# Optimization experiments

Hardware: AMD Instinct MI355X
Metric: run time of the kernel (lower is better)

## Reference

```python
import jax, jax.numpy as jnp
import numpy as np

EMBED_DIM = 1024
NUM_HEADS = 16
HEAD_DIM = EMBED_DIM // NUM_HEADS


def setup_inputs() -> dict:
    key = jax.random.key(0)
    ks = jax.random.split(key, 9)
    B, S, D = 4, 2048, EMBED_DIM
    s = 1.0 / np.sqrt(D)
    return {
        "x": jax.random.normal(ks[0], (B, S, D), dtype=jnp.float32),
        "Wq": jax.random.uniform(ks[1], (D, D), jnp.float32, -s, s),
        "bq": jax.random.uniform(ks[2], (D,), jnp.float32, -s, s),
        "Wk": jax.random.uniform(ks[3], (D, D), jnp.float32, -s, s),
        "bk": jax.random.uniform(ks[4], (D,), jnp.float32, -s, s),
        "Wv": jax.random.uniform(ks[5], (D, D), jnp.float32, -s, s),
        "bv": jax.random.uniform(ks[6], (D,), jnp.float32, -s, s),
        "Wo": jax.random.uniform(ks[7], (D, D), jnp.float32, -s, s),
        "bo": jax.random.uniform(ks[8], (D,), jnp.float32, -s, s),
    }


def reference(x, Wq, bq, Wk, bk, Wv, bv, Wo, bo):
    B, S, D = x.shape
    H, Hd = NUM_HEADS, HEAD_DIM

    def proj(W, b):
        # torch Linear: x @ W.T + b; reshape to [B, H, S, Hd]
        y = jnp.einsum('bsd,ed->bse', x, W) + b
        return y.reshape(B, S, H, Hd).transpose(0, 2, 1, 3)

    Q = proj(Wq, bq)
    K = proj(Wk, bk)
    V = proj(Wv, bv)
    scores = jnp.einsum('bhqd,bhkd->bhqk', Q, K) / np.sqrt(Hd).astype(jnp.float32)
    attn = jax.nn.softmax(scores, axis=-1)
    out = jnp.einsum('bhqk,bhkd->bhqd', attn, V)
    out = out.transpose(0, 2, 1, 3).reshape(B, S, D)
    return jnp.einsum('bsd,ed->bse', out, Wo) + bo
```

## Files before the change

### kernel.cpp

```cpp
#include <hip/hip_runtime.h>
#include <stdint.h>

typedef unsigned short u16;
typedef _Float16 f16;
typedef __fp16 fp16x2 __attribute__((ext_vector_type(2)));
typedef f16 f16x8 __attribute__((ext_vector_type(8)));
typedef float f32x4 __attribute__((ext_vector_type(4)));
typedef u16 u16x8v __attribute__((ext_vector_type(8)));
typedef uint32_t u32x4 __attribute__((ext_vector_type(4)));

#define MFMAH __builtin_amdgcn_mfma_f32_16x16x32_f16

__device__ __forceinline__ void gload16(const void* g, void* l) {
    __builtin_amdgcn_global_load_lds(
        (const __attribute__((address_space(1))) uint32_t*)g,
        (__attribute__((address_space(3))) uint32_t*)l, 16, 0, 0);
}

__global__ __launch_bounds__(256) void convert_x(const float4* __restrict__ x,
                                                 f16x8* __restrict__ o) {
    int i = blockIdx.x * 256 + threadIdx.x;
    float4 a = x[2 * i], b = x[2 * i + 1];
    f16x8 h;
    h[0] = (f16)a.x; h[1] = (f16)a.y; h[2] = (f16)a.z; h[3] = (f16)a.w;
    h[4] = (f16)b.x; h[5] = (f16)b.y; h[6] = (f16)b.z; h[7] = (f16)b.w;
    o[i] = h;
}

__global__ __launch_bounds__(256) void convert_w(const float4* __restrict__ Wq,
                                                 const float4* __restrict__ Wk,
                                                 const float4* __restrict__ Wv,
                                                 const float4* __restrict__ Wo,
                                                 f16x8* __restrict__ hi,
                                                 f16x8* __restrict__ lo) {
    int gi = blockIdx.x * 256 + threadIdx.x;
    int wsel = gi >> 17;
    int li = gi & 131071;
    const float4* src = (wsel == 0) ? Wq : (wsel == 1) ? Wk : (wsel == 2) ? Wv : Wo;
    float4 a = src[2 * li], b = src[2 * li + 1];
    float v[8] = {a.x, a.y, a.z, a.w, b.x, b.y, b.z, b.w};
    f16x8 h;
#pragma unroll
    for (int j = 0; j < 8; ++j) h[j] = (f16)v[j];
    hi[gi] = h;
    if (wsel == 3) {
        f16x8 l;
#pragma unroll
        for (int j = 0; j < 8; ++j) l[j] = (f16)(v[j] - (float)h[j]);
        lo[gi] = l;
    }
}

__global__ __launch_bounds__(512, 4)
void gemm_qkv(const f16* __restrict__ A,
              const f16* __restrict__ Whi,
              const float* __restrict__ b0, const float* __restrict__ b1,
              const float* __restrict__ b2,
              f16* __restrict__ oq, f16* __restrict__ ok, f16* __restrict__ ov) {
    __shared__ f16 ldsA[256 * 64];
    __shared__ f16 ldsW[128 * 64];
    const int t = threadIdx.x;
    const int lane = t & 63, quad = lane >> 4, l16 = lane & 15;
    const int wid = t >> 6;
    const int wsel = blockIdx.x >> 3;
    const int bm = blockIdx.y * 256;
    const int bn = (blockIdx.x & 7) * 128;
    const int wm = (wid >> 1) * 64, wn = (wid & 1) * 64;
    const f16* Wh = Whi + (size_t)wsel * 1048576;
    const float* bias = (wsel == 0) ? b0 : (wsel == 1) ? b1 : b2;

    f32x4 acc[4][4] = {};

    for (int kt = 0; kt < 16; ++kt) {
        __syncthreads();
        const int k0 = kt * 64;
#pragma unroll
        for (int c = 0; c < 4; ++c) {
            const int u = c * 512 + t;
            const int r = u >> 3, cc = u & 7;
            const int sc = cc ^ (r & 7);
            gload16(A + (size_t)(bm + r) * 1024 + k0 + sc * 8, &ldsA[u * 8]);
        }
#pragma unroll
        for (int c = 0; c < 2; ++c) {
            const int u = c * 512 + t;
            const int r = u >> 3, cc = u & 7;
            const int sc = cc ^ (r & 7);
            gload16(Wh + (size_t)(bn + r) * 1024 + k0 + sc * 8, &ldsW[u * 8]);
        }
        __syncthreads();

#pragma unroll
        for (int kq = 0; kq < 2; ++kq) {
            f16x8 bh[4];
            const int chb = kq * 4 + quad;
            const int ch = chb ^ (l16 & 7);
#pragma unroll
            for (int i = 0; i < 4; ++i) {
                const int rb = wn + i * 16 + l16;
                bh[i] = *(const f16x8*)&ldsW[rb * 64 + ch * 8];
            }
#pragma unroll
            for (int mi = 0; mi < 4; ++mi) {
                const int ra = wm + mi * 16 + l16;
                const f16x8 af = *(const f16x8*)&ldsA[ra * 64 + ch * 8];
#pragma unroll
                for (int ni = 0; ni < 4; ++ni)
                    acc[mi][ni] = MFMAH(af, bh[ni], acc[mi][ni], 0, 0, 0);
            }
        }
    }

#pragma unroll
    for (int ni = 0; ni < 4; ++ni) {
        const int e = bn + wn + ni * 16 + l16;
        const float bv = bias[e];
        const int h = e >> 6, d = e & 63;
#pragma unroll
        for (int mi = 0; mi < 4; ++mi) {
            const int row0 = bm + wm + mi * 16 + quad * 4;
            if (wsel == 2) {
                const int b = row0 >> 11, s0 = row0 & 2047;
                ushort4 pk;
                f16 p0 = (f16)(acc[mi][ni][0] + bv);
                f16 p1 = (f16)(acc[mi][ni][1] + bv);
                f16 p2 = (f16)(acc[mi][ni][2] + bv);
                f16 p3 = (f16)(acc[mi][ni][3] + bv);
                pk.x = __builtin_bit_cast(u16, p0);
                pk.y = __builtin_bit_cast(u16, p1);
                pk.z = __builtin_bit_cast(u16, p2);
                pk.w = __builtin_bit_cast(u16, p3);
                *(ushort4*)(ov + ((size_t)((b * 16 + h) * 64 + d)) * 2048 + s0) = pk;
            } else {
                f16* dst = (wsel == 0) ? oq : ok;
#pragma unroll
                for (int r = 0; r < 4; ++r) {
                    const int row = row0 + r;
                    const int b = row >> 11, s = row & 2047;
                    float v = acc[mi][ni][r] + bv;
                    if (wsel == 0) v *= 0.18033688f;
                    dst[((size_t)((b * 16 + h) * 2048 + s)) * 64 + d] = (f16)v;
                }
            }
        }
    }
}

__global__ __launch_bounds__(256, 2)
void gemm_o(const f16* __restrict__ A,
            const f16* __restrict__ Wh, const f16* __restrict__ Wl,
            const float* __restrict__ bias, float* __restrict__ ofp) {
    __shared__ f16 ldsA[128 * 64];
    __shared__ f16 ldsW[2][128 * 64];
    const int t = threadIdx.x;
    const int lane = t & 63, quad = lane >> 4, l16 = lane & 15;
    const int wid = t >> 6;
    const int bm = blockIdx.y * 128, bn = blockIdx.x * 128;
    const int wm = (wid >> 1) * 64, wn = (wid & 1) * 64;

    f32x4 acc[4][4] = {};

    for (int kt = 0; kt < 16; ++kt) {
        __syncthreads();
        const int k0 = kt * 64;
#pragma unroll
        for (int c = 0; c < 4; ++c) {
            const int u = c * 256 + t;
            const int r = u >> 3, cc = u & 7;
            const int sc = cc ^ (r & 7);
            gload16(A + (size_t)(bm + r) * 1024 + k0 + sc * 8, &ldsA[u * 8]);
        }
#pragma unroll
        for (int p = 0; p < 2; ++p) {
            const f16* Ws = p ? Wl : Wh;
#pragma unroll
            for (int c = 0; c < 4; ++c) {
                const int u = c * 256 + t;
                const int r = u >> 3, cc = u & 7;
                const int sc = cc ^ (r & 7);
                gload16(Ws + (size_t)(bn + r) * 1024 + k0 + sc * 8, &ldsW[p][u * 8]);
            }
        }
        __syncthreads();

#pragma unroll
        for (int kq = 0; kq < 2; ++kq) {
            f16x8 bh[4], bl[4];
            const int ch = (kq * 4 + quad) ^ (l16 & 7);
#pragma unroll
            for (int i = 0; i < 4; ++i) {
                const int rb = wn + i * 16 + l16;
                bh[i] = *(const f16x8*)&ldsW[0][rb * 64 + ch * 8];
                bl[i] = *(const f16x8*)&ldsW[1][rb * 64 + ch * 8];
            }
#pragma unroll
            for (int mi = 0; mi < 4; ++mi) {
                const int ra = wm + mi * 16 + l16;
                const f16x8 af = *(const f16x8*)&ldsA[ra * 64 + ch * 8];
#pragma unroll
                for (int ni = 0; ni < 4; ++ni) {
                    acc[mi][ni] = MFMAH(af, bh[ni], acc[mi][ni], 0, 0, 0);
                    acc[mi][ni] = MFMAH(af, bl[ni], acc[mi][ni], 0, 0, 0);
                }
            }
        }
    }

#pragma unroll
    for (int ni = 0; ni < 4; ++ni) {
        const int e = bn + wn + ni * 16 + l16;
        const float bv = bias[e];
#pragma unroll
        for (int mi = 0; mi < 4; ++mi) {
            const int row0 = bm + wm + mi * 16 + quad * 4;
#pragma unroll
            for (int r = 0; r < 4; ++r)
                ofp[(size_t)(row0 + r) * 1024 + e] = acc[mi][ni][r] + bv;
        }
    }
}

__global__ __launch_bounds__(256, 4)
void attn_fused(const f16* __restrict__ Q, const f16* __restrict__ K,
                const f16* __restrict__ Vt, f16* __restrict__ AO) {
    __shared__ f16 Kt[128 * 64];
    __shared__ f16 Vs[64 * 128];
    const int t = threadIdx.x, wid = t >> 6, lane = t & 63;
    const int quad = lane >> 4, l16 = lane & 15;
    const int sw7 = l16 & 7;
    const int bh = blockIdx.x;
    const int q0 = blockIdx.y * 128;
    const size_t base = (size_t)bh * (2048 * 64);

    const u16x8v ou = {0x3C00, 0x3C00, 0x3C00, 0x3C00, 0x3C00, 0x3C00, 0x3C00, 0x3C00};
    const f16x8 ONES = __builtin_bit_cast(f16x8, ou);

    const int idxA = (((quad & 1) << 5) + l16) << 2;
    const int idxB = idxA + 64;
    const bool loPlane = quad < 2;

    f16x8 qf[2][2];
#pragma unroll
    for (int s = 0; s < 2; ++s) {
        const int qrow = q0 + wid * 32 + s * 16 + l16;
        qf[s][0] = *(const f16x8*)(Q + base + (size_t)qrow * 64 + quad * 8);
        qf[s][1] = *(const f16x8*)(Q + base + (size_t)qrow * 64 + 32 + quad * 8);
    }

    f32x4 of[2][4] = {};
    f32x4 rs[2] = {};

    for (int kt = 0; kt < 16; ++kt) {
        __syncthreads();
#pragma unroll
        for (int c = 0; c < 4; ++c) {
            const int u = c * 256 + t;
            const int row = u >> 3, cc = u & 7;
            const int sc = cc ^ (row & 7);
            gload16(K + base + (size_t)(kt * 128 + row) * 64 + sc * 8, &Kt[u * 8]);
        }
#pragma unroll
        for (int c = 0; c < 4; ++c) {
            const int u = c * 256 + t;
            const int row = u >> 4, cc = u & 15;
            const int sc = cc ^ (row & 15);
            gload16(Vt + base + (size_t)row * 2048 + kt * 128 + sc * 8, &Vs[u * 8]);
        }
        __syncthreads();

#pragma unroll
        for (int kk = 0; kk < 4; ++kk) {
            int xp[2][2][2];
#pragma unroll
            for (int nn = 0; nn < 2; ++nn) {
                const int row = (kk * 2 + nn) * 16 + l16;
                const f16x8 kb0 = *(const f16x8*)&Kt[row * 64 + (quad ^ sw7) * 8];
                const f16x8 kb1 = *(const f16x8*)&Kt[row * 64 + ((4 | quad) ^ sw7) * 8];
#pragma unroll
                for (int s = 0; s < 2; ++s) {
                    f32x4 sf = {};
                    sf = MFMAH(kb0, qf[s][0], sf, 0, 0, 0);
                    sf = MFMAH(kb1, qf[s][1], sf, 0, 0, 0);
                    const float p0 = __builtin_amdgcn_exp2f(sf[0]);
                    const float p1 = __builtin_amdgcn_exp2f(sf[1]);
                    const float p2 = __builtin_amdgcn_exp2f(sf[2]);
                    const float p3 = __builtin_amdgcn_exp2f(sf[3]);
                    xp[nn][s][0] = __builtin_bit_cast(int, __builtin_amdgcn_cvt_pkrtz(p0, p1));
                    xp[nn][s][1] = __builtin_bit_cast(int, __builtin_amdgcn_cvt_pkrtz(p2, p3));
                }
            }
            f16x8 pf[2];
#pragma unroll
            for (int s = 0; s < 2; ++s) {
                const int qa00 = __builtin_amdgcn_ds_bpermute(idxA, xp[0][s][0]);
                const int qa01 = __builtin_amdgcn_ds_bpermute(idxA, xp[0][s][1]);
                const int qa10 = __builtin_amdgcn_ds_bpermute(idxA, xp[1][s][0]);
                const int qa11 = __builtin_amdgcn_ds_bpermute(idxA, xp[1][s][1]);
                const int qb00 = __builtin_amdgcn_ds_bpermute(idxB, xp[0][s][0]);
                const int qb01 = __builtin_amdgcn_ds_bpermute(idxB, xp[0][s][1]);
                const int qb10 = __builtin_amdgcn_ds_bpermute(idxB, xp[1][s][0]);
                const int qb11 = __builtin_amdgcn_ds_bpermute(idxB, xp[1][s][1]);
                const uint32_t dw0 = (uint32_t)(loPlane ? qa00 : qa10);
                const uint32_t dw1 = (uint32_t)(loPlane ? qa01 : qa11);
                const uint32_t dw2 = (uint32_t)(loPlane ? qb00 : qb10);
                const uint32_t dw3 = (uint32_t)(loPlane ? qb01 : qb11);
                u32x4 pw = {dw0, dw1, dw2, dw3};
                pf[s] = __builtin_bit_cast(f16x8, pw);
            }
#pragma unroll
            for (int di = 0; di < 4; ++di) {
                const int row = di * 16 + l16;
                const f16x8 vb = *(const f16x8*)&Vs[row * 128 + ((kk * 4 + quad) ^ l16) * 8];
#pragma unroll
                for (int s = 0; s < 2; ++s)
                    of[s][di] = MFMAH(vb, pf[s], of[s][di], 0, 0, 0);
            }
#pragma unroll
            for (int s = 0; s < 2; ++s)
                rs[s] = MFMAH(ONES, pf[s], rs[s], 0, 0, 0);
        }
    }

    const int b = bh >> 4, h = bh & 15;
#pragma unroll
    for (int s = 0; s < 2; ++s) {
        const int qrow = q0 + wid * 32 + s * 16 + l16;
        const float inv = 1.0f / rs[s][0];
#pragma unroll
        for (int di = 0; di < 4; ++di) {
            const int e0 = h * 64 + di * 16 + quad * 4;
            ushort4 pk;
            f16 o0 = (f16)(of[s][di][0] * inv);
            f16 o1 = (f16)(of[s][di][1] * inv);
            f16 o2 = (f16)(of[s][di][2] * inv);
            f16 o3 = (f16)(of[s][di][3] * inv);
            pk.x = __builtin_bit_cast(u16, o0);
            pk.y = __builtin_bit_cast(u16, o1);
            pk.z = __builtin_bit_cast(u16, o2);
            pk.w = __builtin_bit_cast(u16, o3);
            *(ushort4*)(AO + (size_t)(b * 2048 + qrow) * 1024 + e0) = pk;
        }
    }
}

extern "C" void kernel_launch(void* const* d_in, const int* in_sizes, int n_in,
                              void* d_out, int out_size, void* d_ws, size_t ws_size,
                              hipStream_t stream) {
    const float* x  = (const float*)d_in[0];
    const float* Wq = (const float*)d_in[1];
    const float* bq = (const float*)d_in[2];
    const float* Wk = (const float*)d_in[3];
    const float* bk = (const float*)d_in[4];
    const float* Wv = (const float*)d_in[5];
    const float* bv = (const float*)d_in[6];
    const float* Wo = (const float*)d_in[7];
    const float* bo = (const float*)d_in[8];
    float* out = (float*)d_out;

    char* ws = (char*)d_ws;
    f16* XF  = (f16*)(ws);
    f16* WH  = (f16*)(ws + (16u << 20));
    f16* WL  = (f16*)(ws + (24u << 20));
    f16* QF  = (f16*)(ws + (32u << 20));
    f16* KF  = (f16*)(ws + (48u << 20));
    f16* VTF = (f16*)(ws + (64u << 20));
    f16* AOF = (f16*)(ws + (80u << 20));

    convert_x<<<4096, 256, 0, stream>>>((const float4*)x, (f16x8*)XF);
    convert_w<<<2048, 256, 0, stream>>>((const float4*)Wq, (const float4*)Wk,
                                        (const float4*)Wv, (const float4*)Wo,
                                        (f16x8*)WH, (f16x8*)WL);

    gemm_qkv<<<dim3(24, 32), 512, 0, stream>>>(XF, WH, bq, bk, bv, QF, KF, VTF);

    attn_fused<<<dim3(64, 16), 256, 0, stream>>>(QF, KF, VTF, AOF);

    gemm_o<<<dim3(8, 64), 256, 0, stream>>>(AOF, WH + 3145728, WL + 3145728, bo, out);
}
```

Before: 293.8 us.

## Double-buffer K/V tiles, widen attention blocks, and drop bpermute via 16x16x16 MFMA

The attention kernel now uses double-buffered K and V tiles in shared memory, prefetching the next tile while the current one is computed, which hides load latency and removes one barrier per step. Blocks grow to 512 threads covering 256 queries, so each loaded K/V tile is reused by twice as many queries. The ds_bpermute lane shuffle that rearranged P into the 16x16x32 MFMA layout is removed by using 16x16x16 MFMAs that take the score output layout directly. The trade-off is twice as many MFMA issues for the PV and rowsum products, double the LDS footprint (32KB per block), and fewer blocks in the grid.

```diff
diff --git a/kernel.cpp b/kernel.cpp
--- a/kernel.cpp
+++ b/kernel.cpp
@@ -4,12 +4,14 @@
 typedef unsigned short u16;
 typedef _Float16 f16;
 typedef __fp16 fp16x2 __attribute__((ext_vector_type(2)));
+typedef f16 f16x4 __attribute__((ext_vector_type(4)));
 typedef f16 f16x8 __attribute__((ext_vector_type(8)));
 typedef float f32x4 __attribute__((ext_vector_type(4)));
-typedef u16 u16x8v __attribute__((ext_vector_type(8)));
-typedef uint32_t u32x4 __attribute__((ext_vector_type(4)));
-
-#define MFMAH __builtin_amdgcn_mfma_f32_16x16x32_f16
+typedef u16 u16x4v __attribute__((ext_vector_type(4)));
+typedef uint32_t u32x2 __attribute__((ext_vector_type(2)));
+
+#define MFMAH  __builtin_amdgcn_mfma_f32_16x16x32_f16
+#define MFMA16 __builtin_amdgcn_mfma_f32_16x16x16f16
 
 __device__ __forceinline__ void gload16(const void* g, void* l) {
     __builtin_amdgcn_global_load_lds(
@@ -220,24 +222,20 @@
     }
 }
 
-__global__ __launch_bounds__(256, 4)
+__global__ __launch_bounds__(512, 4)
 void attn_fused(const f16* __restrict__ Q, const f16* __restrict__ K,
                 const f16* __restrict__ Vt, f16* __restrict__ AO) {
-    __shared__ f16 Kt[128 * 64];
-    __shared__ f16 Vs[64 * 128];
+    __shared__ f16 Kt[2][128 * 64];
+    __shared__ f16 Vs[2][64 * 128];
     const int t = threadIdx.x, wid = t >> 6, lane = t & 63;
     const int quad = lane >> 4, l16 = lane & 15;
     const int sw7 = l16 & 7;
     const int bh = blockIdx.x;
-    const int q0 = blockIdx.y * 128;
+    const int q0 = blockIdx.y * 256;
     const size_t base = (size_t)bh * (2048 * 64);
 
-    const u16x8v ou = {0x3C00, 0x3C00, 0x3C00, 0x3C00, 0x3C00, 0x3C00, 0x3C00, 0x3C00};
-    const f16x8 ONES = __builtin_bit_cast(f16x8, ou);
-
-    const int idxA = (((quad & 1) << 5) + l16) << 2;
-    const int idxB = idxA + 64;
-    const bool loPlane = quad < 2;
+    const u16x4v o4 = {0x3C00, 0x3C00, 0x3C00, 0x3C00};
+    const f16x4 ONES4 = __builtin_bit_cast(f16x4, o4);
 
     f16x8 qf[2][2];
 #pragma unroll
@@ -250,32 +248,38 @@
     f32x4 of[2][4] = {};
     f32x4 rs[2] = {};
 
-    for (int kt = 0; kt < 16; ++kt) {
-        __syncthreads();
-#pragma unroll
-        for (int c = 0; c < 4; ++c) {
-            const int u = c * 256 + t;
+    auto STAGE = [&](int bf, int kt) {
+#pragma unroll
+        for (int c = 0; c < 2; ++c) {
+            const int u = c * 512 + t;
             const int row = u >> 3, cc = u & 7;
             const int sc = cc ^ (row & 7);
-            gload16(K + base + (size_t)(kt * 128 + row) * 64 + sc * 8, &Kt[u * 8]);
-        }
-#pragma unroll
-        for (int c = 0; c < 4; ++c) {
-            const int u = c * 256 + t;
+            gload16(K + base + (size_t)(kt * 128 + row) * 64 + sc * 8, &Kt[bf][u * 8]);
+        }
+#pragma unroll
+        for (int c = 0; c < 2; ++c) {
+            const int u = c * 512 + t;
             const int row = u >> 4, cc = u & 15;
             const int sc = cc ^ (row & 15);
-            gload16(Vt + base + (size_t)row * 2048 + kt * 128 + sc * 8, &Vs[u * 8]);
-        }
-        __syncthreads();
+            gload16(Vt + base + (size_t)row * 2048 + kt * 128 + sc * 8, &Vs[bf][u * 8]);
+        }
+    };
+
+    STAGE(0, 0);
+    __syncthreads();
+
+    for (int kt = 0; kt < 16; ++kt) {
+        const int bf = kt & 1;
+        if (kt < 15) STAGE(bf ^ 1, kt + 1);
 
 #pragma unroll
         for (int kk = 0; kk < 4; ++kk) {
-            int xp[2][2][2];
+            f16x4 pfq[2][2];
 #pragma unroll
             for (int nn = 0; nn < 2; ++nn) {
-                const int row = (kk * 2 + nn) * 16 + l16;
-                const f16x8 kb0 = *(const f16x8*)&Kt[row * 64 + (quad ^ sw7) * 8];
-                const f16x8 kb1 = *(const f16x8*)&Kt[row * 64 + ((4 | quad) ^ sw7) * 8];
+                const int krow = (kk * 2 + nn) * 16 + l16;
+                const f16x8 kb0 = *(const f16x8*)&Kt[bf][krow * 64 + (quad ^ sw7) * 8];
+                const f16x8 kb1 = *(const f16x8*)&Kt[bf][krow * 64 + ((4 | quad) ^ sw7) * 8];
 #pragma unroll
                 for (int s = 0; s < 2; ++s) {
                     f32x4 sf = {};
@@ -285,40 +289,32 @@
                     const float p1 = __builtin_amdgcn_exp2f(sf[1]);
                     const float p2 = __builtin_amdgcn_exp2f(sf[2]);
                     const float p3 = __builtin_amdgcn_exp2f(sf[3]);
-                    xp[nn][s][0] = __builtin_bit_cast(int, __builtin_amdgcn_cvt_pkrtz(p0, p1));
-                    xp[nn][s][1] = __builtin_bit_cast(int, __builtin_amdgcn_cvt_pkrtz(p2, p3));
+                    u32x2 pw;
+                    pw[0] = __builtin_bit_cast(uint32_t, __builtin_amdgcn_cvt_pkrtz(p0, p1));
+                    pw[1] = __builtin_bit_cast(uint32_t, __builtin_amdgcn_cvt_pkrtz(p2, p3));
+                    pfq[nn][s] = __builtin_bit_cast(f16x4, pw);
                 }
-            }
-            f16x8 pf[2];
-#pragma unroll
-            for (int s = 0; s < 2; ++s) {
-                const int qa00 = __builtin_amdgcn_ds_bpermute(idxA, xp[0][s][0]);
-                const int qa01 = __builtin_amdgcn_ds_bpermute(idxA, xp[0][s][1]);
-                const int qa10 = __builtin_amdgcn_ds_bpermute(idxA, xp[1][s][0]);
-                const int qa11 = __builtin_amdgcn_ds_bpermute(idxA, xp[1][s][1]);
-                const int qb00 = __builtin_amdgcn_ds_bpermute(idxB, xp[0][s][0]);
-                const int qb01 = __builtin_amdgcn_ds_bpermute(idxB, xp[0][s][1]);
-                const int qb10 = __builtin_amdgcn_ds_bpermute(idxB, xp[1][s][0]);
-                const int qb11 = __builtin_amdgcn_ds_bpermute(idxB, xp[1][s][1]);
-                const uint32_t dw0 = (uint32_t)(loPlane ? qa00 : qa10);
-                const uint32_t dw1 = (uint32_t)(loPlane ? qa01 : qa11);
-                const uint32_t dw2 = (uint32_t)(loPlane ? qb00 : qb10);
-                const uint32_t dw3 = (uint32_t)(loPlane ? qb01 : qb11);
-                u32x4 pw = {dw0, dw1, dw2, dw3};
-                pf[s] = __builtin_bit_cast(f16x8, pw);
             }
 #pragma unroll
             for (int di = 0; di < 4; ++di) {
                 const int row = di * 16 + l16;
-                const f16x8 vb = *(const f16x8*)&Vs[row * 128 + ((kk * 4 + quad) ^ l16) * 8];
+#pragma unroll
+                for (int nn = 0; nn < 2; ++nn) {
+                    const int col = kk * 32 + nn * 16 + quad * 4;
+                    const int chunk = (col >> 3) ^ (row & 15);
+                    const f16x4 vb4 = *(const f16x4*)&Vs[bf][row * 128 + chunk * 8 + (quad & 1) * 4];
+#pragma unroll
+                    for (int s = 0; s < 2; ++s)
+                        of[s][di] = MFMA16(vb4, pfq[nn][s], of[s][di], 0, 0, 0);
+                }
+            }
+#pragma unroll
+            for (int nn = 0; nn < 2; ++nn)
 #pragma unroll
                 for (int s = 0; s < 2; ++s)
-                    of[s][di] = MFMAH(vb, pf[s], of[s][di], 0, 0, 0);
-            }
-#pragma unroll
-            for (int s = 0; s < 2; ++s)
-                rs[s] = MFMAH(ONES, pf[s], rs[s], 0, 0, 0);
-        }
+                    rs[s] = MFMA16(ONES4, pfq[nn][s], rs[s], 0, 0, 0);
+        }
+        __syncthreads();
     }
 
     const int b = bh >> 4, h = bh & 15;
@@ -373,7 +369,7 @@
 
     gemm_qkv<<<dim3(24, 32), 512, 0, stream>>>(XF, WH, bq, bk, bv, QF, KF, VTF);
 
-    attn_fused<<<dim3(64, 16), 256, 0, stream>>>(QF, KF, VTF, AOF);
+    attn_fused<<<dim3(64, 8), 512, 0, stream>>>(QF, KF, VTF, AOF);
 
     gemm_o<<<dim3(8, 64), 256, 0, stream>>>(AOF, WH + 3145728, WL + 3145728, bo, out);
 }
```

New measurement: 284.6 us. -3.1%, faster.
